# Performance work log

Measured on AMD Instinct MI355X. Metric: run time of the kernel, lower is better.

The kernel has to match this reference:

```python
import jax, jax.numpy as jnp
import numpy as np
import math

B, S, D = 4, 4096, 2048
HEAD_DIM = 128  # dim_model // head_nums = 2048 // 16
DEPTH = 12


def setup_inputs() -> dict:
    key = jax.random.key(0)
    ks = jax.random.split(key, 8)
    std = 0.1
    return {
        "x": jax.random.normal(ks[0], (B, S, D), dtype=jnp.float32),
        "WQ": jax.random.normal(ks[1], (D, 2 * HEAD_DIM), dtype=jnp.float32) * (D ** -0.5),
        "WK": jax.random.normal(ks[2], (D, 2 * HEAD_DIM), dtype=jnp.float32) * (D ** -0.5),
        "WV": jax.random.normal(ks[3], (D, 2 * HEAD_DIM), dtype=jnp.float32) * (D ** -0.5),
        "lambda_q1": jax.random.normal(ks[4], (HEAD_DIM,), dtype=jnp.float32) * std,
        "lambda_q2": jax.random.normal(ks[5], (HEAD_DIM,), dtype=jnp.float32) * std,
        "lambda_k1": jax.random.normal(ks[6], (HEAD_DIM,), dtype=jnp.float32) * std,
        "lambda_k2": jax.random.normal(ks[7], (HEAD_DIM,), dtype=jnp.float32) * std,
    }


def reference(x, WQ, WK, WV, lambda_q1, lambda_q2, lambda_k1, lambda_k2):
    scale = HEAD_DIM ** -0.5
    lambda_init = 0.8 - 0.6 * math.exp(-0.3 * DEPTH)

    q = x @ WQ                      # [B, S, 2*hd]
    k = x @ WK
    v = x @ WV                      # [B, S, 2*hd]
    q1, q2 = q[..., :HEAD_DIM], q[..., HEAD_DIM:]
    k1, k2 = k[..., :HEAD_DIM], k[..., HEAD_DIM:]

    a1 = jnp.einsum("bqd,bkd->bqk", q1, k1) * scale  # [B, S, S]
    a2 = jnp.einsum("bqd,bkd->bqk", q2, k2) * scale

    lambda_1 = jnp.exp(jnp.sum(lambda_q1 * lambda_k1))
    lambda_2 = jnp.exp(jnp.sum(lambda_q2 * lambda_k2))
    lam = lambda_1 + lambda_2 + lambda_init

    attn = jax.nn.softmax(a1, axis=-1) - lam * jax.nn.softmax(a2, axis=-1)
    return jnp.einsum("bqk,bkd->bqd", attn, v)  # [B, S, 2*hd]
```

## Files before the change

### kernel.cpp

```cpp
#include <hip/hip_runtime.h>
#include <stdint.h>

typedef unsigned short u16;
typedef __attribute__((ext_vector_type(4))) float f32x4;
typedef __attribute__((ext_vector_type(16))) float f32x16;
typedef __attribute__((ext_vector_type(8))) short s16x8;
typedef __attribute__((ext_vector_type(8))) __bf16 bf16x8;
typedef __attribute__((ext_vector_type(8))) unsigned short u16x8;
typedef __attribute__((ext_vector_type(4))) unsigned short u16x4;
typedef __attribute__((ext_vector_type(4))) uint32_t u32x4;
typedef __attribute__((ext_vector_type(2))) uint32_t u32x2;

__device__ __forceinline__ f32x4 mfma16(s16x8 a, s16x8 b, f32x4 c) {
  return __builtin_amdgcn_mfma_f32_16x16x32_bf16(
      __builtin_bit_cast(bf16x8, a), __builtin_bit_cast(bf16x8, b), c, 0, 0, 0);
}
__device__ __forceinline__ f32x16 mfma32(s16x8 a, s16x8 b, f32x16 c) {
  return __builtin_amdgcn_mfma_f32_32x32x16_bf16(
      __builtin_bit_cast(bf16x8, a), __builtin_bit_cast(bf16x8, b), c, 0, 0, 0);
}

__device__ __forceinline__ void gl_lds16(const u16* g, u16* l) {
  __builtin_amdgcn_global_load_lds(
      (const __attribute__((address_space(1))) void*)g,
      (__attribute__((address_space(3))) void*)l, 16, 0, 0);
}

__device__ __forceinline__ u16 bf16rne(float f) {
  uint32_t u = __builtin_bit_cast(uint32_t, f);
  u += 0x7fffu + ((u >> 16) & 1u);
  return (u16)(u >> 16);
}

__global__ void cast_x_kernel(const float* __restrict__ x, u16* __restrict__ xb) {
  size_t i = ((size_t)blockIdx.x * 256 + threadIdx.x) * 8;
  f32x4 a = *(const f32x4*)(x + i);
  f32x4 b = *(const f32x4*)(x + i + 4);
  u16x8 o;
#pragma unroll
  for (int j = 0; j < 4; ++j) { o[j] = bf16rne(a[j]); o[4 + j] = bf16rne(b[j]); }
  *(u16x8*)(xb + i) = o;
}

__global__ void cast_w_kernel(const float* __restrict__ WQ, const float* __restrict__ WK,
                              const float* __restrict__ WV, u16* __restrict__ Wt, float qscale) {
  int i = blockIdx.x * 256 + threadIdx.x;
  int r = i >> 11, k = i & 2047;
  int sel = r >> 8, c = r & 255;
  const float* W = (sel == 0) ? WQ : (sel == 1) ? WK : WV;
  float v = W[(size_t)k * 256 + c];
  if (sel == 0) v *= qscale;
  Wt[i] = bf16rne(v);
}

__global__ __launch_bounds__(256) void proj_gemm(const u16* __restrict__ xb, const u16* __restrict__ Wt,
                                                 u16* __restrict__ Qb, u16* __restrict__ Kb,
                                                 u16* __restrict__ Vt) {
  const int bid = blockIdx.x;
  const int xcd = bid & 7, j = bid >> 3;
  const int m0 = (xcd * 16 + (j / 6)) * 128;
  const int n0 = (j % 6) * 128;
  const int tid = threadIdx.x, lane = tid & 63, w = tid >> 6;
  const int ln = lane & 15, quad = lane >> 4;
  const int wm = w & 1, wn = w >> 1;
  __shared__ __align__(16) u16 As[2][128 * 32];
  __shared__ __align__(16) u16 Bs[2][128 * 32];
  f32x4 acc[4][4];
#pragma unroll
  for (int i = 0; i < 4; ++i)
#pragma unroll
    for (int jj = 0; jj < 4; ++jj) acc[i][jj] = f32x4{0.f, 0.f, 0.f, 0.f};

  auto stage = [&](int kk, int bi) {
#pragma unroll
    for (int i = 0; i < 2; ++i) {
      int p = tid + i * 256;
      int row = p >> 2, cg = (p & 3) ^ (row & 3);
      gl_lds16(xb + (size_t)(m0 + row) * 2048 + kk + cg * 8, As[bi] + (size_t)(p - lane) * 8);
      gl_lds16(Wt + (size_t)(n0 + row) * 2048 + kk + cg * 8, Bs[bi] + (size_t)(p - lane) * 8);
    }
  };

  stage(0, 0);
  for (int t = 0; t < 64; ++t) {
    __syncthreads();
    if (t + 1 < 64) stage((t + 1) * 32, (t + 1) & 1);
    const u16* Asb = As[t & 1];
    const u16* Bsb = Bs[t & 1];
    s16x8 a[4];
#pragma unroll
    for (int mt = 0; mt < 4; ++mt) {
      int r = wm * 64 + mt * 16 + ln;
      a[mt] = *(const s16x8*)(Asb + r * 32 + ((quad ^ (r & 3)) * 8));
    }
#pragma unroll
    for (int nt = 0; nt < 4; ++nt) {
      int r = wn * 64 + nt * 16 + ln;
      s16x8 bf = *(const s16x8*)(Bsb + r * 32 + ((quad ^ (r & 3)) * 8));
#pragma unroll
      for (int mt = 0; mt < 4; ++mt) acc[mt][nt] = mfma16(a[mt], bf, acc[mt][nt]);
    }
  }
#pragma unroll
  for (int mt = 0; mt < 4; ++mt)
#pragma unroll
    for (int nt = 0; nt < 4; ++nt) {
      int row0 = m0 + wm * 64 + mt * 16 + quad * 4;
      int col = n0 + wn * 64 + nt * 16 + ln;
      int sel = col >> 8, c = col & 255;
      u16x4 vv;
#pragma unroll
      for (int jj = 0; jj < 4; ++jj) vv[jj] = bf16rne(acc[mt][nt][jj]);
      if (sel == 2) {
        int b = row0 >> 12, s = row0 & 4095;
        *(u16x4*)(Vt + (size_t)b * 1048576 + (size_t)c * 4096 + s) = vv;
      } else {
        u16* dst = (sel == 0) ? Qb : Kb;
#pragma unroll
        for (int jj = 0; jj < 4; ++jj) dst[(size_t)(row0 + jj) * 256 + c] = vv[jj];
      }
    }
}

__global__ void lam_kernel(const float* __restrict__ lq1, const float* __restrict__ lq2,
                           const float* __restrict__ lk1, const float* __restrict__ lk2,
                           float* __restrict__ lamp) {
  int t = threadIdx.x;
  float d1 = lq1[t] * lk1[t] + lq1[t + 64] * lk1[t + 64];
  float d2 = lq2[t] * lk2[t] + lq2[t + 64] * lk2[t + 64];
#pragma unroll
  for (int off = 32; off; off >>= 1) {
    d1 += __shfl_xor(d1, off);
    d2 += __shfl_xor(d2, off);
  }
  if (t == 0) *lamp = expf(d1) + expf(d2) + (0.8f - 0.6f * expf(-3.6f));
}

__global__ __launch_bounds__(512, 2) void attn_kernel(const u16* __restrict__ Qb,
                                                      const u16* __restrict__ Kb,
                                                      const u16* __restrict__ Vt,
                                                      const float* __restrict__ lamp,
                                                      float* __restrict__ out) {
  const int bid = blockIdx.x;
  const int xcd = bid & 7;
  const int b = xcd >> 1;
  const int qt = ((bid >> 3) << 1) + (xcd & 1);
  const int tid = threadIdx.x, lane = tid & 63, w = tid >> 6;
  const int l5 = lane & 31, lh = lane >> 5;
  const int m = w & 1, kt = (w >> 1) & 1, qh = w >> 2;

  __shared__ __align__(16) char smem[134144];
  float* buf0 = (float*)smem;
  float* buf1 = (float*)(smem + 66560);
  float* ls = (float*)(smem + 133120);

  const u16* Kg0 = Kb + ((size_t)b * 4096) * 256;
  const u16* Vg0 = Vt + (size_t)b * 1048576;

  auto stage = [&](int kb, char* base) {
    u16* Ks = (u16*)base;
    u16* Vs = (u16*)(base + 32768);
#pragma unroll
    for (int i = 0; i < 4; ++i) {
      int p = tid + i * 512;
      int row = p >> 5, c = p & 31;
      int cg = (c & 16) | ((c ^ row) & 15);
      gl_lds16(Kg0 + (size_t)(kb + row) * 256 + cg * 8, Ks + (size_t)(p - lane) * 8);
    }
#pragma unroll
    for (int i = 0; i < 4; ++i) {
      int p = tid + i * 512;
      int row = p >> 3, c = p & 7;
      int cg = c ^ (row & 7);
      gl_lds16(Vg0 + (size_t)row * 4096 + kb + cg * 8, Vs + (size_t)(p - lane) * 8);
    }
  };

  stage(0, smem);

  s16x8 bq[8];
  {
    const u16* qp =
        Qb + ((size_t)(b * 4096 + qt * 64 + qh * 32 + l5)) * 256 + m * 128 + lh * 8;
#pragma unroll
    for (int s = 0; s < 8; ++s) bq[s] = *(const s16x8*)(qp + s * 16);
  }

  f32x16 O[8];
#pragma unroll
  for (int ct = 0; ct < 8; ++ct)
#pragma unroll
    for (int r = 0; r < 16; ++r) O[ct][r] = 0.f;
  float l_run = 0.f;

  for (int t = 0; t < 64; ++t) {
    __syncthreads();
    if (t + 1 < 64) stage((t + 1) * 64, smem + ((t + 1) & 1) * 65536);

    char* base = smem + (t & 1) * 65536;
    u16* Ks = (u16*)base;
    u16* Vs = (u16*)(base + 32768);

    f32x16 Sa, Sb;
#pragma unroll
    for (int r = 0; r < 16; ++r) { Sa[r] = 0.f; Sb[r] = 0.f; }
#pragma unroll
    for (int s = 0; s < 8; s += 2) {
      int row = kt * 32 + l5;
      int c0 = m * 16 + s * 2 + lh;
      int c1 = m * 16 + (s + 1) * 2 + lh;
      s16x8 a0 = *(const s16x8*)(Ks + row * 256 + (((c0 & 16) | ((c0 ^ row) & 15))) * 8);
      s16x8 a1 = *(const s16x8*)(Ks + row * 256 + (((c1 & 16) | ((c1 ^ row) & 15))) * 8);
      Sa = mfma32(a0, bq[s], Sa);
      Sb = mfma32(a1, bq[s + 1], Sb);
    }

    s16x8 vfr0[8], vfr1[8];
#pragma unroll
    for (int ct = 0; ct < 8; ++ct) {
      int row = ct * 32 + l5;
      int c0v = (kt * 32) / 8 + lh;
      int c1v = (kt * 32 + 16) / 8 + lh;
      vfr0[ct] = *(const s16x8*)(Vs + row * 64 + ((c0v ^ (row & 7)) * 8));
      vfr1[ct] = *(const s16x8*)(Vs + row * 64 + ((c1v ^ (row & 7)) * 8));
    }

    uint32_t P[8];
#pragma unroll
    for (int d = 0; d < 8; ++d) {
      float p0 = __builtin_amdgcn_exp2f(Sa[2 * d] + Sb[2 * d]);
      float p1 = __builtin_amdgcn_exp2f(Sa[2 * d + 1] + Sb[2 * d + 1]);
      l_run += p0 + p1;
      P[d] = (uint32_t)bf16rne(p0) | ((uint32_t)bf16rne(p1) << 16);
    }

#pragma unroll
    for (int ks = 0; ks < 2; ++ks) {
      u32x2 s02 = __builtin_amdgcn_permlane32_swap(P[ks * 4 + 0], P[ks * 4 + 2], false, false);
      u32x2 s13 = __builtin_amdgcn_permlane32_swap(P[ks * 4 + 1], P[ks * 4 + 3], false, false);
      u32x4 fd;
      fd[0] = s02[0]; fd[1] = s13[0]; fd[2] = s02[1]; fd[3] = s13[1];
      s16x8 pf = __builtin_bit_cast(s16x8, fd);
      if (ks == 0) {
#pragma unroll
        for (int ct = 0; ct < 8; ++ct) O[ct] = mfma32(vfr0[ct], pf, O[ct]);
      } else {
#pragma unroll
        for (int ct = 0; ct < 8; ++ct) O[ct] = mfma32(vfr1[ct], pf, O[ct]);
      }
    }
  }

  float lam = *lamp;
  l_run += __shfl_xor(l_run, 32);
  __syncthreads();
  if (lane < 32) ls[w * 32 + l5] = l_run;
  float* bufm = m ? buf1 : buf0;
  const int qb0 = qh * 32;
  if (kt == 1) {
#pragma unroll
    for (int ct = 0; ct < 8; ++ct)
#pragma unroll
      for (int r = 0; r < 16; ++r) {
        int vcol = ct * 32 + (r & 3) + 8 * (r >> 2) + 4 * lh;
        bufm[vcol * 65 + qb0 + l5] = O[ct][r];
      }
  }
  __syncthreads();
  if (kt == 0) {
    float linv = 1.f / (ls[w * 32 + l5] + ls[(w | 2) * 32 + l5]);
#pragma unroll
    for (int ct = 0; ct < 8; ++ct)
#pragma unroll
      for (int r = 0; r < 16; ++r) {
        int vcol = ct * 32 + (r & 3) + 8 * (r >> 2) + 4 * lh;
        bufm[vcol * 65 + qb0 + l5] = (O[ct][r] + bufm[vcol * 65 + qb0 + l5]) * linv;
      }
  }
  __syncthreads();
  float* og = out + ((size_t)(b * 4096 + qt * 64)) * 256;
  const int col = tid & 255, half = tid >> 8;
#pragma unroll
  for (int j2 = 0; j2 < 32; ++j2) {
    int q = half * 32 + j2;
    float v = buf0[col * 65 + q] - lam * buf1[col * 65 + q];
    og[(size_t)q * 256 + col] = v;
  }
}

extern "C" void kernel_launch(void* const* d_in, const int* in_sizes, int n_in,
                              void* d_out, int out_size, void* d_ws, size_t ws_size,
                              hipStream_t stream) {
  (void)in_sizes; (void)n_in; (void)out_size; (void)ws_size;
  const float* x   = (const float*)d_in[0];
  const float* WQ  = (const float*)d_in[1];
  const float* WK  = (const float*)d_in[2];
  const float* WV  = (const float*)d_in[3];
  const float* lq1 = (const float*)d_in[4];
  const float* lq2 = (const float*)d_in[5];
  const float* lk1 = (const float*)d_in[6];
  const float* lk2 = (const float*)d_in[7];
  float* out = (float*)d_out;

  char* ws = (char*)d_ws;
  u16* xb = (u16*)ws;   ws += (size_t)16384 * 2048 * 2;
  u16* Wt = (u16*)ws;   ws += (size_t)768 * 2048 * 2;
  u16* Qb = (u16*)ws;   ws += (size_t)16384 * 256 * 2;
  u16* Kb = (u16*)ws;   ws += (size_t)16384 * 256 * 2;
  u16* Vt = (u16*)ws;   ws += (size_t)16384 * 256 * 2;
  float* lamp = (float*)ws;

  const float qscale = 0.0883883476f * 1.44269504f;

  hipLaunchKernelGGL(cast_x_kernel, dim3(16384), dim3(256), 0, stream, x, xb);
  hipLaunchKernelGGL(cast_w_kernel, dim3(6144), dim3(256), 0, stream, WQ, WK, WV, Wt, qscale);
  hipLaunchKernelGGL(proj_gemm, dim3(768), dim3(256), 0, stream, xb, Wt, Qb, Kb, Vt);
  hipLaunchKernelGGL(lam_kernel, dim3(1), dim3(64), 0, stream, lq1, lq2, lk1, lk2, lamp);
  hipLaunchKernelGGL(attn_kernel, dim3(256), dim3(512), 0, stream, Qb, Kb, Vt, lamp, out);
}
```

Baseline: 393.5 us.

## Fuse fp32-to-bf16 cast of x into projection GEMM A-tile staging

Removes the separate cast_x kernel and the bf16 copy of x in the workspace. The projection GEMM now loads fp32 x into registers, converts it to bf16, and writes it to LDS after the MFMA loop, so the next tile's load overlaps with compute. This drops a full read and write pass over x (128MB read, 64MB written and reread). In exchange the GEMM reads twice as many bytes for A, uses more registers, and loses the async global_load_lds path for A. Each of the 6 N-tile blocks per M-row now rereads fp32 x instead of bf16.

New measurement: 405.1 us. +2.9%, slower.

```diff
diff --git a/kernel.cpp b/kernel.cpp
--- a/kernel.cpp
+++ b/kernel.cpp
@@ -32,16 +32,6 @@
   return (u16)(u >> 16);
 }
 
-__global__ void cast_x_kernel(const float* __restrict__ x, u16* __restrict__ xb) {
-  size_t i = ((size_t)blockIdx.x * 256 + threadIdx.x) * 8;
-  f32x4 a = *(const f32x4*)(x + i);
-  f32x4 b = *(const f32x4*)(x + i + 4);
-  u16x8 o;
-#pragma unroll
-  for (int j = 0; j < 4; ++j) { o[j] = bf16rne(a[j]); o[4 + j] = bf16rne(b[j]); }
-  *(u16x8*)(xb + i) = o;
-}
-
 __global__ void cast_w_kernel(const float* __restrict__ WQ, const float* __restrict__ WK,
                               const float* __restrict__ WV, u16* __restrict__ Wt, float qscale) {
   int i = blockIdx.x * 256 + threadIdx.x;
@@ -53,7 +43,7 @@
   Wt[i] = bf16rne(v);
 }
 
-__global__ __launch_bounds__(256) void proj_gemm(const u16* __restrict__ xb, const u16* __restrict__ Wt,
+__global__ __launch_bounds__(256) void proj_gemm(const float* __restrict__ x, const u16* __restrict__ Wt,
                                                  u16* __restrict__ Qb, u16* __restrict__ Kb,
                                                  u16* __restrict__ Vt) {
   const int bid = blockIdx.x;
@@ -71,20 +61,50 @@
 #pragma unroll
     for (int jj = 0; jj < 4; ++jj) acc[i][jj] = f32x4{0.f, 0.f, 0.f, 0.f};
 
-  auto stage = [&](int kk, int bi) {
+  auto stageB = [&](int kk, int bi) {
 #pragma unroll
     for (int i = 0; i < 2; ++i) {
       int p = tid + i * 256;
       int row = p >> 2, cg = (p & 3) ^ (row & 3);
-      gl_lds16(xb + (size_t)(m0 + row) * 2048 + kk + cg * 8, As[bi] + (size_t)(p - lane) * 8);
       gl_lds16(Wt + (size_t)(n0 + row) * 2048 + kk + cg * 8, Bs[bi] + (size_t)(p - lane) * 8);
     }
   };
 
-  stage(0, 0);
+  f32x4 areg[2][2];
+  auto loadA = [&](int kk) {
+#pragma unroll
+    for (int i = 0; i < 2; ++i) {
+      int p = tid + i * 256;
+      int row = p >> 2, cg = (p & 3) ^ (row & 3);
+      const float* src = x + (size_t)(m0 + row) * 2048 + kk + cg * 8;
+      areg[i][0] = *(const f32x4*)src;
+      areg[i][1] = *(const f32x4*)(src + 4);
+    }
+  };
+  auto writeA = [&](int bi) {
+#pragma unroll
+    for (int i = 0; i < 2; ++i) {
+      int p = tid + i * 256;
+      u16x8 o;
+#pragma unroll
+      for (int jj = 0; jj < 4; ++jj) {
+        o[jj] = __builtin_bit_cast(u16, (__bf16)areg[i][0][jj]);
+        o[4 + jj] = __builtin_bit_cast(u16, (__bf16)areg[i][1][jj]);
+      }
+      *(u16x8*)(As[bi] + (size_t)p * 8) = o;
+    }
+  };
+
+  stageB(0, 0);
+  loadA(0);
+  writeA(0);
+
   for (int t = 0; t < 64; ++t) {
     __syncthreads();
-    if (t + 1 < 64) stage((t + 1) * 32, (t + 1) & 1);
+    if (t + 1 < 64) {
+      loadA((t + 1) * 32);
+      stageB((t + 1) * 32, (t + 1) & 1);
+    }
     const u16* Asb = As[t & 1];
     const u16* Bsb = Bs[t & 1];
     s16x8 a[4];
@@ -100,6 +120,7 @@
 #pragma unroll
       for (int mt = 0; mt < 4; ++mt) acc[mt][nt] = mfma16(a[mt], bf, acc[mt][nt]);
     }
+    if (t + 1 < 64) writeA((t + 1) & 1);
   }
 #pragma unroll
   for (int mt = 0; mt < 4; ++mt)
@@ -303,7 +324,6 @@
   float* out = (float*)d_out;
 
   char* ws = (char*)d_ws;
-  u16* xb = (u16*)ws;   ws += (size_t)16384 * 2048 * 2;
   u16* Wt = (u16*)ws;   ws += (size_t)768 * 2048 * 2;
   u16* Qb = (u16*)ws;   ws += (size_t)16384 * 256 * 2;
   u16* Kb = (u16*)ws;   ws += (size_t)16384 * 256 * 2;
@@ -312,9 +332,8 @@
 
   const float qscale = 0.0883883476f * 1.44269504f;
 
-  hipLaunchKernelGGL(cast_x_kernel, dim3(16384), dim3(256), 0, stream, x, xb);
   hipLaunchKernelGGL(cast_w_kernel, dim3(6144), dim3(256), 0, stream, WQ, WK, WV, Wt, qscale);
-  hipLaunchKernelGGL(proj_gemm, dim3(768), dim3(256), 0, stream, xb, Wt, Qb, Kb, Vt);
+  hipLaunchKernelGGL(proj_gemm, dim3(768), dim3(256), 0, stream, x, Wt, Qb, Kb, Vt);
   hipLaunchKernelGGL(lam_kernel, dim3(1), dim3(64), 0, stream, lq1, lq2, lk1, lk2, lamp);
   hipLaunchKernelGGL(attn_kernel, dim3(256), dim3(512), 0, stream, Qb, Kb, Vt, lamp, out);
 }
```
